# Kernel tuning notes

Hardware: AMD Instinct MI355X
Metric: run time of the kernel (lower is better)

Reference implementation:

```python
import jax, jax.numpy as jnp
import numpy as np

B = 8192          # batch of agents
K = 4             # max_neighbors
NUM_LANES = 12
LANE_F = 4        # obs_dim // num_lanes = 48 // 12
HEADS = 4
OUT = 32          # gat_output_dim per head
EMB = HEADS * OUT # 128, gat_per_lane_output / intersection emb dim
HID = 64          # graphsage_hidden_dim
GRU_H = 32        # gru_hidden_dim
ALPHA = 0.2       # leaky relu slope

# Lane cooperation: lanes of the same approach (4 approaches x 3 lanes) cooperate.
_blk = np.kron(np.eye(4), np.ones((3, 3))).astype(np.float32)
LANE_COOP = jnp.asarray(_blk)
LANE_CONF = jnp.asarray(1.0 - _blk)


def _gat_stream(x, W, a_src, a_dst, adj):
    # x: [N, 12, 4]; W: [H, 4, O]; a_*: [H, O]; adj: [12, 12]
    Wh = jnp.einsum('nlf,hfo->nhlo', x, W)                      # [N,H,12,O]
    e_s = jnp.einsum('nhlo,ho->nhl', Wh, a_src)
    e_d = jnp.einsum('nhlo,ho->nhl', Wh, a_dst)
    e = jax.nn.leaky_relu(e_s[..., :, None] + e_d[..., None, :], ALPHA)  # [N,H,12,12]
    e = jnp.where(adj[None, None] > 0, e, jnp.float32(-1e9))
    att = jax.nn.softmax(e, axis=-1)
    out = jnp.einsum('nhij,nhjo->niho', att, Wh)                # [N,12,H,O]
    return jax.nn.elu(out.reshape(out.shape[0], NUM_LANES, EMB))


def _gru_final(xs, Wih, Whh, bih, bhh):
    # xs: [K, B, HID] -> final hidden [B, GRU_H], torch GRU gate convention (r,z,n)
    def step(h, x):
        gi = x @ Wih + bih
        gh = h @ Whh + bhh
        i_r, i_z, i_n = jnp.split(gi, 3, axis=-1)
        h_r, h_z, h_n = jnp.split(gh, 3, axis=-1)
        r = jax.nn.sigmoid(i_r + h_r)
        z = jax.nn.sigmoid(i_z + h_z)
        n = jnp.tanh(i_n + r * h_n)
        return (1.0 - z) * n + z * h, None
    h0 = jnp.zeros((xs.shape[1], Whh.shape[0]), xs.dtype)
    hT, _ = jax.lax.scan(step, h0, xs)
    return hT


def setup_inputs() -> dict:
    key = jax.random.key(0)
    ks = jax.random.split(key, 24)
    rn = lambda k, s: (jax.random.normal(k, s, jnp.float32) * 0.1)
    z = lambda n: jnp.zeros((n,), jnp.float32)
    return {
        'self_features': jax.random.normal(ks[0], (B, 48), jnp.float32),
        'neighbor_features': jax.random.normal(ks[1], (B, K, 48), jnp.float32),
        'neighbor_mask': (jax.random.uniform(ks[2], (B, K)) > 0.25).astype(jnp.float32),
        'neighbor_directions': jax.random.randint(ks[3], (B, K), 0, 4).astype(jnp.float32) * 0.25,
        # dual-stream GAT params
        'W_coop': rn(ks[4], (HEADS, LANE_F, OUT)), 'a_src_coop': rn(ks[5], (HEADS, OUT)), 'a_dst_coop': rn(ks[6], (HEADS, OUT)),
        'W_conf': rn(ks[7], (HEADS, LANE_F, OUT)), 'a_src_conf': rn(ks[8], (HEADS, OUT)), 'a_dst_conf': rn(ks[9], (HEADS, OUT)),
        'W_fuse': rn(ks[10], (2 * EMB, EMB)), 'b_fuse': z(EMB),
        # GraphSAGE neighbor projection (+1 for direction feature)
        'W_proj': rn(ks[11], (EMB + 1, HID)), 'b_proj': z(HID),
        # BiGRU (fwd/bwd), torch layout transposed: Wih [HID,3H], Whh [H,3H]
        'Wih_f': rn(ks[12], (HID, 3 * GRU_H)), 'Whh_f': rn(ks[13], (GRU_H, 3 * GRU_H)), 'bih_f': z(3 * GRU_H), 'bhh_f': z(3 * GRU_H),
        'Wih_b': rn(ks[14], (HID, 3 * GRU_H)), 'Whh_b': rn(ks[15], (GRU_H, 3 * GRU_H)), 'bih_b': z(3 * GRU_H), 'bhh_b': z(3 * GRU_H),
        # combine self + BiGRU summary -> network embedding
        'W_out': rn(ks[16], (EMB + 2 * GRU_H, HID)), 'b_out': z(HID),
    }


def reference(self_features, neighbor_features, neighbor_mask, neighbor_directions,
              W_coop, a_src_coop, a_dst_coop, W_conf, a_src_conf, a_dst_conf,
              W_fuse, b_fuse, W_proj, b_proj,
              Wih_f, Whh_f, bih_f, bhh_f, Wih_b, Whh_b, bih_b, bhh_b,
              W_out, b_out):
    Bc, Kc = neighbor_features.shape[:2]
    # run dual-stream GAT on self + all neighbors in one batch of small lane graphs
    allx = jnp.concatenate([self_features[:, None, :], neighbor_features], axis=1)
    allx = allx.reshape(Bc * (Kc + 1), NUM_LANES, LANE_F)
    coop = _gat_stream(allx, W_coop, a_src_coop, a_dst_coop, LANE_COOP)
    conf = _gat_stream(allx, W_conf, a_src_conf, a_dst_conf, LANE_CONF)
    fused = jax.nn.elu(jnp.concatenate([coop, conf], axis=-1) @ W_fuse + b_fuse)  # [N,12,128]
    emb = fused.mean(axis=1).reshape(Bc, Kc + 1, EMB)  # mean pool over lanes
    self_emb = emb[:, 0]          # [B,128]
    nbr_emb = emb[:, 1:]          # [B,K,128]
    # GraphSAGE projection of neighbors (direction-aware), masked
    nbr_in = jnp.concatenate([nbr_emb, neighbor_directions[..., None]], axis=-1)
    x = jax.nn.relu(nbr_in @ W_proj + b_proj) * neighbor_mask[..., None]  # [B,K,HID]
    xs = jnp.swapaxes(x, 0, 1)    # [K,B,HID]
    h_f = _gru_final(xs, Wih_f, Whh_f, bih_f, bhh_f)
    h_b = _gru_final(xs[::-1], Wih_b, Whh_b, bih_b, bhh_b)
    net = jax.nn.relu(jnp.concatenate([self_emb, h_f, h_b], axis=-1) @ W_out + b_out)  # [B,64]
    return jnp.concatenate([self_emb, net], axis=-1)  # [B,192]
```

## Files before the change

kernel.cpp:

```cpp
#include <hip/hip_runtime.h>
#include <hip/hip_bf16.h>
#include <math.h>

typedef short short8 __attribute__((ext_vector_type(8)));
typedef float f32x4  __attribute__((ext_vector_type(4)));

__device__ __forceinline__ unsigned short f2b(float f) {
  union { float f; unsigned int u; } x; x.f = f;
  return (unsigned short)((x.u + 0x7FFFu + ((x.u >> 16) & 1u)) >> 16);
}
__device__ __forceinline__ float b2f_u(unsigned short u) {
  union { unsigned int u; float f; } x; x.u = ((unsigned int)u) << 16;
  return x.f;
}
__device__ __forceinline__ unsigned int pkbf(float a, float b) {
  union { __hip_bfloat162 h; unsigned int u; } c;
  c.h = __float22bfloat162_rn(make_float2(a, b));
  return c.u;
}
__device__ __forceinline__ float sigm(float x) {
  return __builtin_amdgcn_rcpf(1.f + __expf(-x));
}
__device__ __forceinline__ float tanhfast(float x) {
  float ax = fabsf(x);
  float em = __expf(-2.f * ax);
  float t  = (1.f - em) * __builtin_amdgcn_rcpf(1.f + em);
  return copysignf(t, x);
}
__device__ __forceinline__ float eluf(float v) {
  return v > 0.f ? v : (__expf(v) - 1.f);
}

__global__ __launch_bounds__(256) void prepack_kernel(
    const float* __restrict__ Wf,
    const float* __restrict__ Wc, const float* __restrict__ Wn,
    const float* __restrict__ as_c, const float* __restrict__ ad_c,
    const float* __restrict__ as_n, const float* __restrict__ ad_n,
    const float* __restrict__ Wproj,
    const float* __restrict__ Wih_f, const float* __restrict__ Wih_b,
    const float* __restrict__ Wout,
    const float* __restrict__ Whh_f, const float* __restrict__ Whh_b,
    unsigned short* __restrict__ fragB,
    unsigned short* __restrict__ fragWB,
    float* __restrict__ Wa,
    unsigned short* __restrict__ fragP,
    unsigned short* __restrict__ fragIH,
    unsigned short* __restrict__ fragO,
    unsigned short* __restrict__ fragHH)
{
  int e = blockIdx.x * 256 + threadIdx.x;
  unsigned short tmp[8];
  if (e < 4096) {
    int kb = e >> 9, tile = (e >> 6) & 7, lane = e & 63;
    int n = tile * 16 + (lane & 15);
    int kbase = kb * 32 + (lane >> 4) * 8;
#pragma unroll
    for (int j = 0; j < 8; j++) tmp[j] = f2b(Wf[(kbase + j) * 128 + n]);
    *(short8*)(fragB + e * 8) = *(short8*)tmp;
  } else if (e < 5120) {
    int i = e - 4096;
    int s = i >> 9, tile = (i >> 6) & 7, lane = i & 63;
    int c15 = lane & 15, quad = lane >> 4;
    int n = tile * 16 + c15;
    int h = n >> 5, o = n & 31;
    const float* W = s ? Wn : Wc;
#pragma unroll
    for (int j = 0; j < 8; j++) {
      int k = quad * 8 + j;
      tmp[j] = ((k >> 2) == h) ? f2b(W[h * 128 + (k & 3) * 32 + o])
                               : (unsigned short)0;
    }
    *(short8*)(fragWB + i * 8) = *(short8*)tmp;
  } else if (e < 5184) {
    int i = e - 5120;
    int s = i >> 5, d = (i >> 4) & 1, h = (i >> 2) & 3, f = i & 3;
    const float* W = s ? Wn : Wc;
    const float* a = s ? (d ? ad_n : as_n) : (d ? ad_c : as_c);
    float acc = 0.f;
#pragma unroll
    for (int o = 0; o < 32; o++) acc += W[h * 128 + f * 32 + o] * a[h * 32 + o];
    Wa[i] = acc;
  } else if (e < 6208) {
    int i = e - 5184;
    int kb = i >> 8, nt = (i >> 6) & 3, lane = i & 63;
    int c15 = lane & 15, quad = lane >> 4;
#pragma unroll
    for (int j = 0; j < 8; j++)
      tmp[j] = f2b(Wproj[(kb * 32 + quad * 8 + j) * 64 + nt * 16 + c15]);
    *(short8*)(fragP + i * 8) = *(short8*)tmp;
  } else if (e < 7744) {
    int i = e - 6208;
    int d = (i >= 768), r = i - d * 768;
    int kb = r / 384, nt = (r >> 6) % 6, lane = r & 63;
    int c15 = lane & 15, quad = lane >> 4;
    const float* W = d ? Wih_b : Wih_f;
#pragma unroll
    for (int j = 0; j < 8; j++)
      tmp[j] = f2b(W[(kb * 32 + quad * 8 + j) * 96 + nt * 16 + c15]);
    *(short8*)(fragIH + i * 8) = *(short8*)tmp;
  } else if (e < 9280) {
    int r = e - 7744;
    int kb = r >> 8, nt = (r >> 6) & 3, lane = r & 63;
    int c15 = lane & 15, quad = lane >> 4;
#pragma unroll
    for (int j = 0; j < 8; j++)
      tmp[j] = f2b(Wout[(kb * 32 + quad * 8 + j) * 64 + nt * 16 + c15]);
    *(short8*)(fragO + r * 8) = *(short8*)tmp;
  } else if (e < 10048) {
    int i = e - 9280;
    int d = i / 384, r = i - d * 384;
    int nt = r >> 6, lane = r & 63;
    int c15 = lane & 15, quad = lane >> 4;
    const float* W = d ? Whh_b : Whh_f;
#pragma unroll
    for (int j = 0; j < 8; j++)
      tmp[j] = f2b(W[(quad * 8 + j) * 96 + nt * 16 + c15]);
    *(short8*)(fragHH + i * 8) = *(short8*)tmp;
  }
}

__global__ __launch_bounds__(256) void gat_fuse_kernel(
    const float* __restrict__ self_f, const float* __restrict__ nbr_f,
    const float* __restrict__ Wa,
    const unsigned short* __restrict__ fragWB,
    const unsigned short* __restrict__ fragB,
    const float* __restrict__ b_fuse,
    unsigned short* __restrict__ embb,
    float* __restrict__ out)
{
  const int tid = threadIdx.x;
  const int w = tid >> 6, lane = tid & 63, c15 = lane & 15, quad = lane >> 4;
  const int n0 = blockIdx.x * 2;

  __shared__ __align__(16) float sxf[2][12][4];
  __shared__ __align__(16) float sWa[64];
  __shared__ float sed[2][2][4][12];
  __shared__ __align__(16) unsigned short sA[2][2][16][24];
  __shared__ __align__(16) unsigned short scatb[2][16][268];
  __shared__ __align__(16) float sbias[128];

  if (tid < 32) ((f32x4*)sbias)[tid] = ((const f32x4*)b_fuse)[tid];
  else if (tid < 48) ((f32x4*)sWa)[tid - 32] = ((const f32x4*)Wa)[tid - 32];
  if (tid < 24) {
    int nd = (tid >= 12), q = tid - nd * 12;
    int nn = n0 + nd, b = nn / 5, slot = nn - b * 5;
    const float* src = slot ? (nbr_f + (b * 4 + slot - 1) * 48)
                            : (self_f + b * 48);
    ((f32x4*)&sxf[nd][0][0])[q] = *(const f32x4*)(src + q * 4);
  }
  if (tid >= 128) {
    int t = tid - 128;
    int g = t >> 6, s = (t >> 5) & 1, i = 12 + ((t >> 3) & 3), cp = t & 7;
    *(unsigned int*)&sA[g][s][i][cp * 2] = 0u;
  }
  __syncthreads();

  const int g_q = w & 1, s_q = w >> 1;
  if (lane < 48) {
    int h = lane / 12, i = lane - h * 12;
    f32x4 xv  = *(const f32x4*)&sxf[g_q][i][0];
    f32x4 was = *(const f32x4*)&sWa[s_q * 32 + h * 4];
    f32x4 wad = *(const f32x4*)&sWa[s_q * 32 + 16 + h * 4];
    float es = xv[0]*was[0] + xv[1]*was[1] + xv[2]*was[2] + xv[3]*was[3];
    float ed = xv[0]*wad[0] + xv[1]*wad[1] + xv[2]*wad[2] + xv[3]*wad[3];
    sed[g_q][s_q][h][i] = ed;
    int blk3 = (i / 3) * 3;
    float xa0 = 0.f, xa1 = 0.f, xa2 = 0.f, xa3 = 0.f, sum = 0.f;
    if (s_q == 0) {
#pragma unroll
      for (int jj = 0; jj < 3; jj++) {
        int j = blk3 + jj;
        float e = es + sed[g_q][0][h][j];
        e = e > 0.f ? e : 0.2f * e;
        float p = __expf(e);
        sum += p;
        f32x4 xj = *(const f32x4*)&sxf[g_q][j][0];
        xa0 += p * xj[0]; xa1 += p * xj[1];
        xa2 += p * xj[2]; xa3 += p * xj[3];
      }
    } else {
#pragma unroll
      for (int jj = 0; jj < 9; jj++) {
        int j = jj < blk3 ? jj : jj + 3;
        float e = es + sed[g_q][1][h][j];
        e = e > 0.f ? e : 0.2f * e;
        float p = __expf(e);
        sum += p;
        f32x4 xj = *(const f32x4*)&sxf[g_q][j][0];
        xa0 += p * xj[0]; xa1 += p * xj[1];
        xa2 += p * xj[2]; xa3 += p * xj[3];
      }
    }
    float inv = 1.f / sum;
    uint2 pk = make_uint2(pkbf(xa0 * inv, xa1 * inv),
                          pkbf(xa2 * inv, xa3 * inv));
    *(uint2*)&sA[g_q][s_q][i][h * 4] = pk;
  }

  {
    const int wn3 = w & 1, ws3 = w >> 1;
    const short8 z8 = {0,0,0,0,0,0,0,0};
    short8 xb = z8;
    if (quad < 2) xb = *(const short8*)&sA[wn3][ws3][c15][quad * 8];
#pragma unroll
    for (int tile = 0; tile < 8; tile++) {
      short8 aw = *(const short8*)(fragWB + ((ws3 * 8 + tile) * 64 + lane) * 8);
      f32x4 c = {0.f, 0.f, 0.f, 0.f};
      c = __builtin_amdgcn_mfma_f32_16x16x32_bf16(aw, xb, c, 0, 0, 0);
      uint2 pk = make_uint2(pkbf(eluf(c[0]), eluf(c[1])),
                            pkbf(eluf(c[2]), eluf(c[3])));
      *(uint2*)&scatb[wn3][c15][ws3 * 128 + tile * 16 + (quad << 2)] = pk;
    }
  }
  __syncthreads();

  {
    f32x4 acc[2][2];
#pragma unroll
    for (int nd = 0; nd < 2; nd++)
#pragma unroll
      for (int tt = 0; tt < 2; tt++) acc[nd][tt] = (f32x4){0.f,0.f,0.f,0.f};
#pragma unroll
    for (int kb = 0; kb < 8; kb++) {
      short8 a0 = *(const short8*)&scatb[0][c15][kb * 32 + (quad << 3)];
      short8 a1 = *(const short8*)&scatb[1][c15][kb * 32 + (quad << 3)];
#pragma unroll
      for (int tt = 0; tt < 2; tt++) {
        short8 bw = *(const short8*)(fragB + ((kb * 8 + 2 * w + tt) * 64 + lane) * 8);
        acc[0][tt] = __builtin_amdgcn_mfma_f32_16x16x32_bf16(a0, bw, acc[0][tt], 0, 0, 0);
        acc[1][tt] = __builtin_amdgcn_mfma_f32_16x16x32_bf16(a1, bw, acc[1][tt], 0, 0, 0);
      }
    }
    float tot[2][2];
#pragma unroll
    for (int nd = 0; nd < 2; nd++) {
#pragma unroll
      for (int tt = 0; tt < 2; tt++) {
        float p = 0.f;
        if (quad < 3) {
          float bcol = sbias[w * 32 + tt * 16 + c15];
#pragma unroll
          for (int r = 0; r < 4; r++) p += eluf(acc[nd][tt][r] + bcol);
        }
        p += __shfl_xor(p, 16);
        p += __shfl_xor(p, 32);
        tot[nd][tt] = p;
      }
    }
    int ndw = quad >> 1, ttw = quad & 1;
    float val = (ndw ? (ttw ? tot[1][1] : tot[1][0])
                     : (ttw ? tot[0][1] : tot[0][0])) * (1.f / 12.f);
    int node = n0 + ndw;
    int col  = w * 32 + ttw * 16 + c15;
    embb[node * 128 + col] = f2b(val);
    int bq = node / 5;
    if (node == bq * 5) out[bq * 192 + col] = val;
  }
}

__global__ __launch_bounds__(256) void head_kernel(
    const unsigned short* __restrict__ embb,
    const float* __restrict__ maskp, const float* __restrict__ dirsp,
    const float* __restrict__ W_proj, const float* __restrict__ b_proj,
    const unsigned short* __restrict__ fragP,
    const unsigned short* __restrict__ fragIH,
    const unsigned short* __restrict__ fragHH,
    const float* __restrict__ bih_f, const float* __restrict__ bhh_f,
    const float* __restrict__ bih_b, const float* __restrict__ bhh_b,
    const unsigned short* __restrict__ fragO,
    const float* __restrict__ b_out,
    float* __restrict__ out)
{
  const int b8 = blockIdx.x * 8;
  const int tid = threadIdx.x;
  const int w = tid >> 6, lane = tid & 63, c15 = lane & 15, quad = lane >> 4;

  __shared__ __align__(16) unsigned short sX[32][72];
  __shared__ __align__(16) unsigned short sgi[2][32][96];
  __shared__ float sH[2][8][32];
  __shared__ __align__(16) unsigned short sHb[2][16][32];
  __shared__ __align__(16) float sgh[2][8][96];
  __shared__ __align__(16) unsigned short sCat[16][200];
  __shared__ __align__(16) float sPB[128];
  __shared__ __align__(16) float sBI[2][96], sBH[2][96];
  __shared__ __align__(16) float sBO[64];

  if (tid < 64) { sPB[tid] = b_proj[tid]; sPB[64 + tid] = W_proj[128 * 64 + tid]; sBO[tid] = b_out[tid]; }
  if (tid < 96) { sBI[0][tid] = bih_f[tid]; sBI[1][tid] = bih_b[tid];
                  sBH[0][tid] = bhh_f[tid]; sBH[1][tid] = bhh_b[tid]; }
  {
    unsigned int* hb = (unsigned int*)sHb;
    hb[tid] = 0u; hb[tid + 256] = 0u;
    float* hz = (float*)sH;
    for (int i = tid; i < 512; i += 256) hz[i] = 0.f;
  }
  __syncthreads();

  {
    const int mt  = w >> 1;
    const int nt0 = (w & 1) * 2;
    const int sloc = mt * 4 + (c15 >> 2);
    const int nbr  = c15 & 3;
    const unsigned short* brow = embb + (((b8 + sloc) * 5) + 1 + nbr) * 128;
    short8 xb[4];
#pragma unroll
    for (int kb = 0; kb < 4; kb++)
      xb[kb] = *(const short8*)(brow + kb * 32 + quad * 8);
    f32x4 acc0 = {0.f,0.f,0.f,0.f}, acc1 = acc0;
#pragma unroll
    for (int kb = 0; kb < 4; kb++) {
      short8 a0 = *(const short8*)(fragP + ((kb * 4 + nt0    ) * 64 + lane) * 8);
      short8 a1 = *(const short8*)(fragP + ((kb * 4 + nt0 + 1) * 64 + lane) * 8);
      acc0 = __builtin_amdgcn_mfma_f32_16x16x32_bf16(a0, xb[kb], acc0, 0, 0, 0);
      acc1 = __builtin_amdgcn_mfma_f32_16x16x32_bf16(a1, xb[kb], acc1, 0, 0, 0);
    }
    const float dirv  = dirsp[(b8 + sloc) * 4 + nbr];
    const float maskv = maskp[(b8 + sloc) * 4 + nbr];
#pragma unroll
    for (int tt = 0; tt < 2; tt++) {
      f32x4 c = tt ? acc1 : acc0;
      int colb = (nt0 + tt) * 16 + (quad << 2);
      f32x4 wp = *(const f32x4*)&sPB[64 + colb];
      f32x4 pb = *(const f32x4*)&sPB[colb];
      float v0 = fmaxf(c[0] + dirv * wp[0] + pb[0], 0.f) * maskv;
      float v1 = fmaxf(c[1] + dirv * wp[1] + pb[1], 0.f) * maskv;
      float v2 = fmaxf(c[2] + dirv * wp[2] + pb[2], 0.f) * maskv;
      float v3 = fmaxf(c[3] + dirv * wp[3] + pb[3], 0.f) * maskv;
      uint2 pk = make_uint2(pkbf(v0, v1), pkbf(v2, v3));
      *(uint2*)&sX[mt * 16 + c15][colb] = pk;
    }
  }
  __syncthreads();

  {
    const int mt  = w >> 1;
    const int ntb = (w & 1) * 3;
    short8 xb0 = *(const short8*)&sX[mt * 16 + c15][quad * 8];
    short8 xb1 = *(const short8*)&sX[mt * 16 + c15][32 + quad * 8];
#pragma unroll
    for (int d = 0; d < 2; d++) {
#pragma unroll
      for (int t2 = 0; t2 < 3; t2++) {
        int nt = ntb + t2;
        f32x4 acc = {0.f,0.f,0.f,0.f};
        short8 a0 = *(const short8*)(fragIH + ((d * 12 +     nt) * 64 + lane) * 8);
        short8 a1 = *(const short8*)(fragIH + ((d * 12 + 6 + nt) * 64 + lane) * 8);
        acc = __builtin_amdgcn_mfma_f32_16x16x32_bf16(a0, xb0, acc, 0, 0, 0);
        acc = __builtin_amdgcn_mfma_f32_16x16x32_bf16(a1, xb1, acc, 0, 0, 0);
        f32x4 bi = *(const f32x4*)&sBI[d][nt * 16 + (quad << 2)];
        uint2 pk = make_uint2(pkbf(acc[0] + bi[0], acc[1] + bi[1]),
                              pkbf(acc[2] + bi[2], acc[3] + bi[3]));
        *(uint2*)&sgi[d][mt * 16 + c15][nt * 16 + (quad << 2)] = pk;
      }
    }
  }
  __syncthreads();

  if (w < 2) {
    const int d = w;
    const int u = lane & 31, sp = lane >> 5;
    for (int step = 0; step < 4; step++) {
      short8 hb = *(const short8*)&sHb[d][c15][quad * 8];
#pragma unroll
      for (int nt = 0; nt < 6; nt++) {
        short8 aw = *(const short8*)(fragHH + ((d * 6 + nt) * 64 + lane) * 8);
        f32x4 c = {0.f,0.f,0.f,0.f};
        c = __builtin_amdgcn_mfma_f32_16x16x32_bf16(aw, hb, c, 0, 0, 0);
        if (c15 < 8)
          *(f32x4*)&sgh[d][c15][nt * 16 + (quad << 2)] = c;
      }
      const int k = d ? (3 - step) : step;
#pragma unroll
      for (int si = 0; si < 4; si++) {
        int s = sp + si * 2;
        int row = s * 4 + k;
        float ghr = sgh[d][s][u]      + sBH[d][u];
        float ghz = sgh[d][s][32 + u] + sBH[d][32 + u];
        float ghn = sgh[d][s][64 + u] + sBH[d][64 + u];
        float r = sigm(b2f_u(sgi[d][row][u]) + ghr);
        float z = sigm(b2f_u(sgi[d][row][32 + u]) + ghz);
        float n = tanhfast(b2f_u(sgi[d][row][64 + u]) + r * ghn);
        float h = (1.f - z) * n + z * sH[d][s][u];
        sH[d][s][u] = h;
        sHb[d][s][u] = f2b(h);
        if (step == 3) sCat[s][128 + d * 32 + u] = f2b(h);
      }
    }
  } else {
    int t = tid - 128;
    int s = t >> 4, c8 = (t & 15) * 8;
    short8 v = *(const short8*)(embb + (b8 + s) * 5 * 128 + c8);
    *(short8*)&sCat[s][c8] = v;
  }
  __syncthreads();

  {
    const int nt = w;
    f32x4 acc = {0.f,0.f,0.f,0.f};
#pragma unroll
    for (int kb = 0; kb < 6; kb++) {
      short8 bb = *(const short8*)&sCat[c15][kb * 32 + quad * 8];
      short8 aw = *(const short8*)(fragO + ((kb * 4 + nt) * 64 + lane) * 8);
      acc = __builtin_amdgcn_mfma_f32_16x16x32_bf16(aw, bb, acc, 0, 0, 0);
    }
    if (c15 < 8) {
      f32x4 bo = *(const f32x4*)&sBO[nt * 16 + (quad << 2)];
      f32x4 v;
      v[0] = fmaxf(acc[0] + bo[0], 0.f);
      v[1] = fmaxf(acc[1] + bo[1], 0.f);
      v[2] = fmaxf(acc[2] + bo[2], 0.f);
      v[3] = fmaxf(acc[3] + bo[3], 0.f);
      *(f32x4*)(out + (b8 + c15) * 192 + 128 + nt * 16 + (quad << 2)) = v;
    }
  }
}

extern "C" void kernel_launch(void* const* d_in, const int* in_sizes, int n_in,
                              void* d_out, int out_size, void* d_ws, size_t ws_size,
                              hipStream_t stream) {
  const float* self_f  = (const float*)d_in[0];
  const float* nbr_f   = (const float*)d_in[1];
  const float* maskp   = (const float*)d_in[2];
  const float* dirsp   = (const float*)d_in[3];
  const float* W_coop  = (const float*)d_in[4];
  const float* as_coop = (const float*)d_in[5];
  const float* ad_coop = (const float*)d_in[6];
  const float* W_conf  = (const float*)d_in[7];
  const float* as_conf = (const float*)d_in[8];
  const float* ad_conf = (const float*)d_in[9];
  const float* W_fuse  = (const float*)d_in[10];
  const float* b_fuse  = (const float*)d_in[11];
  const float* W_proj  = (const float*)d_in[12];
  const float* b_proj  = (const float*)d_in[13];
  const float* Wih_f   = (const float*)d_in[14];
  const float* Whh_f   = (const float*)d_in[15];
  const float* bih_f   = (const float*)d_in[16];
  const float* bhh_f   = (const float*)d_in[17];
  const float* Wih_b   = (const float*)d_in[18];
  const float* Whh_b   = (const float*)d_in[19];
  const float* bih_b   = (const float*)d_in[20];
  const float* bhh_b   = (const float*)d_in[21];
  const float* W_out   = (const float*)d_in[22];
  const float* b_out   = (const float*)d_in[23];

  const int B = in_sizes[0] / 48;
  char* ws = (char*)d_ws;
  unsigned short* fragB  = (unsigned short*)(ws);
  unsigned short* fragWB = (unsigned short*)(ws + 65536);
  float*          Wa     = (float*)(ws + 81920);
  unsigned short* fragP  = (unsigned short*)(ws + 82176);
  unsigned short* fragIH = (unsigned short*)(ws + 98560);
  unsigned short* fragO  = (unsigned short*)(ws + 123136);
  unsigned short* fragHH = (unsigned short*)(ws + 147712);
  unsigned short* embb   = (unsigned short*)(ws + 160000);

  prepack_kernel<<<40, 256, 0, stream>>>(
      W_fuse, W_coop, W_conf, as_coop, ad_coop, as_conf, ad_conf,
      W_proj, Wih_f, Wih_b, W_out, Whh_f, Whh_b,
      fragB, fragWB, Wa, fragP, fragIH, fragO, fragHH);

  gat_fuse_kernel<<<B * 5 / 2, 256, 0, stream>>>(
      self_f, nbr_f, Wa, fragWB, fragB, b_fuse, embb, (float*)d_out);

  head_kernel<<<B / 8, 256, 0, stream>>>(
      embb, maskp, dirsp, W_proj, b_proj, fragP, fragIH, fragHH,
      bih_f, bhh_f, bih_b, bhh_b,
      fragO, b_out, (float*)d_out);
}
```

Baseline: 227.1 us.

## Make GAT kernel persistent with register-resident weights and prefetch; split GRU across four waves

The GAT/fuse kernel changes from one block per node pair to a persistent grid of 768 blocks. Each block loads its MFMA weight fragments into registers once, then loops over a contiguous range of pairs, prefetching the next pair's input features. This removes the repeated per-pair weight loads and block launch cost, at the price of many more registers (launch bounds ask for 3 blocks per CU) and possible load imbalance. The head kernel's GRU recurrence now uses all four waves, two per direction each handling half the rows, and the embedding copy moves earlier.

```diff
diff --git a/kernel.cpp b/kernel.cpp
--- a/kernel.cpp
+++ b/kernel.cpp
@@ -119,18 +119,18 @@
   }
 }
 
-__global__ __launch_bounds__(256) void gat_fuse_kernel(
+__global__ __launch_bounds__(256, 3) void gat_fuse_kernel(
     const float* __restrict__ self_f, const float* __restrict__ nbr_f,
     const float* __restrict__ Wa,
     const unsigned short* __restrict__ fragWB,
     const unsigned short* __restrict__ fragB,
     const float* __restrict__ b_fuse,
     unsigned short* __restrict__ embb,
-    float* __restrict__ out)
+    float* __restrict__ out,
+    int npairs)
 {
   const int tid = threadIdx.x;
   const int w = tid >> 6, lane = tid & 63, c15 = lane & 15, quad = lane >> 4;
-  const int n0 = blockIdx.x * 2;
 
   __shared__ __align__(16) float sxf[2][12][4];
   __shared__ __align__(16) float sWa[64];
@@ -141,120 +141,147 @@
 
   if (tid < 32) ((f32x4*)sbias)[tid] = ((const f32x4*)b_fuse)[tid];
   else if (tid < 48) ((f32x4*)sWa)[tid - 32] = ((const f32x4*)Wa)[tid - 32];
-  if (tid < 24) {
-    int nd = (tid >= 12), q = tid - nd * 12;
-    int nn = n0 + nd, b = nn / 5, slot = nn - b * 5;
-    const float* src = slot ? (nbr_f + (b * 4 + slot - 1) * 48)
-                            : (self_f + b * 48);
-    ((f32x4*)&sxf[nd][0][0])[q] = *(const f32x4*)(src + q * 4);
-  }
   if (tid >= 128) {
     int t = tid - 128;
     int g = t >> 6, s = (t >> 5) & 1, i = 12 + ((t >> 3) & 3), cp = t & 7;
     *(unsigned int*)&sA[g][s][i][cp * 2] = 0u;
   }
-  __syncthreads();
 
   const int g_q = w & 1, s_q = w >> 1;
-  if (lane < 48) {
-    int h = lane / 12, i = lane - h * 12;
-    f32x4 xv  = *(const f32x4*)&sxf[g_q][i][0];
-    f32x4 was = *(const f32x4*)&sWa[s_q * 32 + h * 4];
-    f32x4 wad = *(const f32x4*)&sWa[s_q * 32 + 16 + h * 4];
-    float es = xv[0]*was[0] + xv[1]*was[1] + xv[2]*was[2] + xv[3]*was[3];
-    float ed = xv[0]*wad[0] + xv[1]*wad[1] + xv[2]*wad[2] + xv[3]*wad[3];
-    sed[g_q][s_q][h][i] = ed;
-    int blk3 = (i / 3) * 3;
-    float xa0 = 0.f, xa1 = 0.f, xa2 = 0.f, xa3 = 0.f, sum = 0.f;
-    if (s_q == 0) {
-#pragma unroll
-      for (int jj = 0; jj < 3; jj++) {
-        int j = blk3 + jj;
-        float e = es + sed[g_q][0][h][j];
-        e = e > 0.f ? e : 0.2f * e;
-        float p = __expf(e);
-        sum += p;
-        f32x4 xj = *(const f32x4*)&sxf[g_q][j][0];
-        xa0 += p * xj[0]; xa1 += p * xj[1];
-        xa2 += p * xj[2]; xa3 += p * xj[3];
-      }
-    } else {
-#pragma unroll
-      for (int jj = 0; jj < 9; jj++) {
-        int j = jj < blk3 ? jj : jj + 3;
-        float e = es + sed[g_q][1][h][j];
-        e = e > 0.f ? e : 0.2f * e;
-        float p = __expf(e);
-        sum += p;
-        f32x4 xj = *(const f32x4*)&sxf[g_q][j][0];
-        xa0 += p * xj[0]; xa1 += p * xj[1];
-        xa2 += p * xj[2]; xa3 += p * xj[3];
-      }
-    }
-    float inv = 1.f / sum;
-    uint2 pk = make_uint2(pkbf(xa0 * inv, xa1 * inv),
-                          pkbf(xa2 * inv, xa3 * inv));
-    *(uint2*)&sA[g_q][s_q][i][h * 4] = pk;
-  }
-
-  {
-    const int wn3 = w & 1, ws3 = w >> 1;
-    const short8 z8 = {0,0,0,0,0,0,0,0};
-    short8 xb = z8;
-    if (quad < 2) xb = *(const short8*)&sA[wn3][ws3][c15][quad * 8];
-#pragma unroll
-    for (int tile = 0; tile < 8; tile++) {
-      short8 aw = *(const short8*)(fragWB + ((ws3 * 8 + tile) * 64 + lane) * 8);
-      f32x4 c = {0.f, 0.f, 0.f, 0.f};
-      c = __builtin_amdgcn_mfma_f32_16x16x32_bf16(aw, xb, c, 0, 0, 0);
-      uint2 pk = make_uint2(pkbf(eluf(c[0]), eluf(c[1])),
-                            pkbf(eluf(c[2]), eluf(c[3])));
-      *(uint2*)&scatb[wn3][c15][ws3 * 128 + tile * 16 + (quad << 2)] = pk;
-    }
-  }
-  __syncthreads();
-
-  {
-    f32x4 acc[2][2];
-#pragma unroll
-    for (int nd = 0; nd < 2; nd++)
-#pragma unroll
-      for (int tt = 0; tt < 2; tt++) acc[nd][tt] = (f32x4){0.f,0.f,0.f,0.f};
-#pragma unroll
-    for (int kb = 0; kb < 8; kb++) {
-      short8 a0 = *(const short8*)&scatb[0][c15][kb * 32 + (quad << 3)];
-      short8 a1 = *(const short8*)&scatb[1][c15][kb * 32 + (quad << 3)];
-#pragma unroll
-      for (int tt = 0; tt < 2; tt++) {
-        short8 bw = *(const short8*)(fragB + ((kb * 8 + 2 * w + tt) * 64 + lane) * 8);
-        acc[0][tt] = __builtin_amdgcn_mfma_f32_16x16x32_bf16(a0, bw, acc[0][tt], 0, 0, 0);
-        acc[1][tt] = __builtin_amdgcn_mfma_f32_16x16x32_bf16(a1, bw, acc[1][tt], 0, 0, 0);
-      }
-    }
-    float tot[2][2];
-#pragma unroll
-    for (int nd = 0; nd < 2; nd++) {
-#pragma unroll
-      for (int tt = 0; tt < 2; tt++) {
-        float p = 0.f;
-        if (quad < 3) {
-          float bcol = sbias[w * 32 + tt * 16 + c15];
-#pragma unroll
-          for (int r = 0; r < 4; r++) p += eluf(acc[nd][tt][r] + bcol);
+  short8 wb3[8];
+#pragma unroll
+  for (int t = 0; t < 8; t++)
+    wb3[t] = *(const short8*)(fragWB + ((s_q * 8 + t) * 64 + lane) * 8);
+  short8 wb4[8][2];
+#pragma unroll
+  for (int kb = 0; kb < 8; kb++)
+#pragma unroll
+    for (int tt = 0; tt < 2; tt++)
+      wb4[kb][tt] = *(const short8*)(fragB + ((kb * 8 + 2 * w + tt) * 64 + lane) * 8);
+
+  const int chunk = (npairs + gridDim.x - 1) / gridDim.x;
+  const int start = blockIdx.x * chunk;
+  const int end   = min(npairs, start + chunk);
+  if (start >= end) return;
+
+  f32x4 xr = {0.f, 0.f, 0.f, 0.f};
+  int xnd = 0, xq = 0;
+  if (tid < 24) {
+    xnd = (tid >= 12); xq = tid - xnd * 12;
+    int nn = start * 2 + xnd, b = nn / 5, slot = nn - b * 5;
+    const float* src = slot ? (nbr_f + (b * 4 + slot - 1) * 48)
+                            : (self_f + b * 48);
+    xr = *(const f32x4*)(src + xq * 4);
+  }
+
+  for (int it = start; it < end; ++it) {
+    const int n0 = it * 2;
+    if (tid < 24) ((f32x4*)&sxf[xnd][0][0])[xq] = xr;
+    __syncthreads();
+    if (tid < 24 && it + 1 < end) {
+      int nn = (it + 1) * 2 + xnd, b = nn / 5, slot = nn - b * 5;
+      const float* src = slot ? (nbr_f + (b * 4 + slot - 1) * 48)
+                              : (self_f + b * 48);
+      xr = *(const f32x4*)(src + xq * 4);
+    }
+
+    if (lane < 48) {
+      int h = lane / 12, i = lane - h * 12;
+      f32x4 xv  = *(const f32x4*)&sxf[g_q][i][0];
+      f32x4 was = *(const f32x4*)&sWa[s_q * 32 + h * 4];
+      f32x4 wad = *(const f32x4*)&sWa[s_q * 32 + 16 + h * 4];
+      float es = xv[0]*was[0] + xv[1]*was[1] + xv[2]*was[2] + xv[3]*was[3];
+      float ed = xv[0]*wad[0] + xv[1]*wad[1] + xv[2]*wad[2] + xv[3]*wad[3];
+      sed[g_q][s_q][h][i] = ed;
+      int blk3 = (i / 3) * 3;
+      float xa0 = 0.f, xa1 = 0.f, xa2 = 0.f, xa3 = 0.f, sum = 0.f;
+      if (s_q == 0) {
+#pragma unroll
+        for (int jj = 0; jj < 3; jj++) {
+          int j = blk3 + jj;
+          float e = es + sed[g_q][0][h][j];
+          e = e > 0.f ? e : 0.2f * e;
+          float p = __expf(e);
+          sum += p;
+          f32x4 xj = *(const f32x4*)&sxf[g_q][j][0];
+          xa0 += p * xj[0]; xa1 += p * xj[1];
+          xa2 += p * xj[2]; xa3 += p * xj[3];
         }
-        p += __shfl_xor(p, 16);
-        p += __shfl_xor(p, 32);
-        tot[nd][tt] = p;
-      }
-    }
-    int ndw = quad >> 1, ttw = quad & 1;
-    float val = (ndw ? (ttw ? tot[1][1] : tot[1][0])
-                     : (ttw ? tot[0][1] : tot[0][0])) * (1.f / 12.f);
-    int node = n0 + ndw;
-    int col  = w * 32 + ttw * 16 + c15;
-    embb[node * 128 + col] = f2b(val);
-    int bq = node / 5;
-    if (node == bq * 5) out[bq * 192 + col] = val;
+      } else {
+#pragma unroll
+        for (int jj = 0; jj < 9; jj++) {
+          int j = jj < blk3 ? jj : jj + 3;
+          float e = es + sed[g_q][1][h][j];
+          e = e > 0.f ? e : 0.2f * e;
+          float p = __expf(e);
+          sum += p;
+          f32x4 xj = *(const f32x4*)&sxf[g_q][j][0];
+          xa0 += p * xj[0]; xa1 += p * xj[1];
+          xa2 += p * xj[2]; xa3 += p * xj[3];
+        }
+      }
+      float inv = 1.f / sum;
+      uint2 pk = make_uint2(pkbf(xa0 * inv, xa1 * inv),
+                            pkbf(xa2 * inv, xa3 * inv));
+      *(uint2*)&sA[g_q][s_q][i][h * 4] = pk;
+    }
+
+    {
+      const short8 z8 = {0,0,0,0,0,0,0,0};
+      short8 xb = z8;
+      if (quad < 2) xb = *(const short8*)&sA[g_q][s_q][c15][quad * 8];
+#pragma unroll
+      for (int tile = 0; tile < 8; tile++) {
+        f32x4 c = {0.f, 0.f, 0.f, 0.f};
+        c = __builtin_amdgcn_mfma_f32_16x16x32_bf16(wb3[tile], xb, c, 0, 0, 0);
+        uint2 pk = make_uint2(pkbf(eluf(c[0]), eluf(c[1])),
+                              pkbf(eluf(c[2]), eluf(c[3])));
+        *(uint2*)&scatb[g_q][c15][s_q * 128 + tile * 16 + (quad << 2)] = pk;
+      }
+    }
+    __syncthreads();
+
+    {
+      f32x4 acc[2][2];
+#pragma unroll
+      for (int nd = 0; nd < 2; nd++)
+#pragma unroll
+        for (int tt = 0; tt < 2; tt++) acc[nd][tt] = (f32x4){0.f,0.f,0.f,0.f};
+#pragma unroll
+      for (int kb = 0; kb < 8; kb++) {
+        short8 a0 = *(const short8*)&scatb[0][c15][kb * 32 + (quad << 3)];
+        short8 a1 = *(const short8*)&scatb[1][c15][kb * 32 + (quad << 3)];
+#pragma unroll
+        for (int tt = 0; tt < 2; tt++) {
+          acc[0][tt] = __builtin_amdgcn_mfma_f32_16x16x32_bf16(a0, wb4[kb][tt], acc[0][tt], 0, 0, 0);
+          acc[1][tt] = __builtin_amdgcn_mfma_f32_16x16x32_bf16(a1, wb4[kb][tt], acc[1][tt], 0, 0, 0);
+        }
+      }
+      float tot[2][2];
+#pragma unroll
+      for (int nd = 0; nd < 2; nd++) {
+#pragma unroll
+        for (int tt = 0; tt < 2; tt++) {
+          float p = 0.f;
+          if (quad < 3) {
+            float bcol = sbias[w * 32 + tt * 16 + c15];
+#pragma unroll
+            for (int r = 0; r < 4; r++) p += eluf(acc[nd][tt][r] + bcol);
+          }
+          p += __shfl_xor(p, 16);
+          p += __shfl_xor(p, 32);
+          tot[nd][tt] = p;
+        }
+      }
+      int ndw = quad >> 1, ttw = quad & 1;
+      float val = (ndw ? (ttw ? tot[1][1] : tot[1][0])
+                       : (ttw ? tot[0][1] : tot[0][0])) * (1.f / 12.f);
+      int node = n0 + ndw;
+      int col  = w * 32 + ttw * 16 + c15;
+      embb[node * 128 + col] = f2b(val);
+      int bq = node / 5;
+      if (node == bq * 5) out[bq * 192 + col] = val;
+    }
   }
 }
 
@@ -353,11 +380,18 @@
         *(uint2*)&sgi[d][mt * 16 + c15][nt * 16 + (quad << 2)] = pk;
       }
     }
+    if (tid >= 128) {
+      int t = tid - 128;
+      int s = t >> 4, c8 = (t & 15) * 8;
+      short8 v = *(const short8*)(embb + (b8 + s) * 5 * 128 + c8);
+      *(short8*)&sCat[s][c8] = v;
+    }
   }
   __syncthreads();
 
-  if (w < 2) {
-    const int d = w;
+  {
+    const int d = w >> 1;
+    const int q = w & 1;
     const int u = lane & 31, sp = lane >> 5;
     for (int step = 0; step < 4; step++) {
       short8 hb = *(const short8*)&sHb[d][c15][quad * 8];
@@ -366,13 +400,13 @@
         short8 aw = *(const short8*)(fragHH + ((d * 6 + nt) * 64 + lane) * 8);
         f32x4 c = {0.f,0.f,0.f,0.f};
         c = __builtin_amdgcn_mfma_f32_16x16x32_bf16(aw, hb, c, 0, 0, 0);
-        if (c15 < 8)
+        if ((c15 >> 2) == q)
           *(f32x4*)&sgh[d][c15][nt * 16 + (quad << 2)] = c;
       }
       const int k = d ? (3 - step) : step;
 #pragma unroll
-      for (int si = 0; si < 4; si++) {
-        int s = sp + si * 2;
+      for (int si = 0; si < 2; si++) {
+        int s = q * 4 + sp + si * 2;
         int row = s * 4 + k;
         float ghr = sgh[d][s][u]      + sBH[d][u];
         float ghz = sgh[d][s][32 + u] + sBH[d][32 + u];
@@ -386,11 +420,6 @@
         if (step == 3) sCat[s][128 + d * 32 + u] = f2b(h);
       }
     }
-  } else {
-    int t = tid - 128;
-    int s = t >> 4, c8 = (t & 15) * 8;
-    short8 v = *(const short8*)(embb + (b8 + s) * 5 * 128 + c8);
-    *(short8*)&sCat[s][c8] = v;
   }
   __syncthreads();
 
@@ -459,8 +488,9 @@
       W_proj, Wih_f, Wih_b, W_out, Whh_f, Whh_b,
       fragB, fragWB, Wa, fragP, fragIH, fragO, fragHH);
 
-  gat_fuse_kernel<<<B * 5 / 2, 256, 0, stream>>>(
-      self_f, nbr_f, Wa, fragWB, fragB, b_fuse, embb, (float*)d_out);
+  const int npairs = B * 5 / 2;
+  gat_fuse_kernel<<<768, 256, 0, stream>>>(
+      self_f, nbr_f, Wa, fragWB, fragB, b_fuse, embb, (float*)d_out, npairs);
 
   head_kernel<<<B / 8, 256, 0, stream>>>(
       embb, maskp, dirsp, W_proj, b_proj, fragP, fragIH, fragHH,
```

Result: slower. 233.3 us (+2.8%).
